# Optimization experiments

Hardware: AMD Instinct MI355X
Metric: run time of the kernel (lower is better)

The kernel has to match this reference:

```python
import jax, jax.numpy as jnp
import numpy as np

B, S, IDIM, D, T, DUR_MAX = 32, 512, 256, 256, 4096, 16
EPS = 1e-6
SIGMA_C = 2.0
PAD = 0
LOG_SQRT_2PI = 0.9189385332046727  # 0.5*log(2*pi)


def setup_inputs() -> dict:
    rng = np.random.default_rng(0)
    # durations in [1, DUR_MAX); clip so each row's total length <= T (ragged tails)
    durs = rng.integers(1, DUR_MAX, size=(B, S))
    excl = np.cumsum(durs, axis=-1) - durs
    durs = np.minimum(durs, np.maximum(T - excl, 0))
    # token ids in [1, IDIM) so PAD=0 only appears via explicit padding
    text = rng.integers(1, IDIM, size=(B, S))
    embed = rng.standard_normal((IDIM, D)).astype(np.float32)
    embed[PAD] = 0.0  # padding_idx=0 row is zeros in nn.Embedding
    return {
        "text": jnp.asarray(text, dtype=jnp.int64),
        "durs": jnp.asarray(durs, dtype=jnp.int64),
        "embed": jnp.asarray(embed),
        "total_time": T,
    }


def reference(text, durs, embed, total_time):
    # F.pad(text/durs, [0, 2]) with value 0
    text_p = jnp.pad(text, ((0, 0), (0, 2)), constant_values=PAD)   # [B, S+2]
    durs_p = jnp.pad(durs, ((0, 0), (0, 2)), constant_values=0)     # [B, S+2]
    S2 = text_p.shape[-1]

    cum = jnp.cumsum(durs_p, axis=-1)                               # [B, S+2]
    durs_f = durs_p.astype(jnp.float32)
    # token centers: durs/2 + exclusive cumsum
    c = durs_f / 2.0 + (cum - durs_p).astype(jnp.float32)           # [B, S+2]
    sig = durs_f / SIGMA_C + EPS                                    # [B, S+2]

    t = jnp.arange(total_time, dtype=jnp.float32) + 0.5             # [T]
    z = (t[None, :, None] - c[:, None, :]) / sig[:, None, :]        # [B, T, S+2]
    # Normal(c, sig).log_prob(t).exp()
    w = jnp.exp(-0.5 * z * z - jnp.log(sig)[:, None, :] - LOG_SQRT_2PI)

    # zero weights on pad tokens, then normalize over tokens
    token_pad = (text_p == PAD)                                     # [B, S+2]
    w = jnp.where(token_pad[:, None, :], 0.0, w)
    w = w / (w.sum(-1, keepdims=True) + EPS)

    # frames beyond a row's total duration correspond to pad in `repeats`:
    # zero all weights there, then set the last token column to 1.0
    time_invalid = jnp.arange(total_time)[None, :] >= cum[:, -1:]   # [B, T]
    w = jnp.where(time_invalid[:, :, None], 0.0, w)
    last_col = (jnp.arange(S2) == S2 - 1)
    w = jnp.where(time_invalid[:, :, None] & last_col[None, None, :], 1.0, w)

    emb = embed[text_p]                                             # [B, S+2, D]
    return jnp.einsum("bts,bsd->btd", w, emb)                       # [B, T, D]
```

## Files before the change

kernel.cpp:

```cpp
#include <hip/hip_runtime.h>

#define B_ 32
#define S_ 512
#define D_ 256
#define T_ 4096
#define IDIM_ 256
#define EPS_ 1e-6f
#define INV_SQRT_2PI 0.3989422804014327f
#define NHALF_LOG2E -0.7213475204444817f
#define W_ 28
#define FPW_ 16

typedef float float4n __attribute__((ext_vector_type(4)));

__global__ __launch_bounds__(512) void GaussianEmbedding_prep(
    const int* __restrict__ text, const int* __restrict__ durs,
    float4* __restrict__ toks, int* __restrict__ tof, int* __restrict__ totb)
{
    int b = blockIdx.x;
    int s = threadIdx.x;
    int dur = durs[b * S_ + s];
    int lane = s & 63, wv = s >> 6;

    int incl = dur;
    #pragma unroll
    for (int o = 1; o < 64; o <<= 1) {
        int v = __shfl_up(incl, o);
        if (lane >= o) incl += v;
    }
    __shared__ int wsum[8];
    __shared__ int stot;
    if (lane == 63) wsum[wv] = incl;
    __syncthreads();
    int woff = 0;
    for (int i = 0; i < wv; ++i) woff += wsum[i];
    int excl = woff + incl - dur;

    if (s == 0) {
        int tot = 0;
        for (int i = 0; i < 8; ++i) tot += wsum[i];
        totb[b] = tot;
        stot = tot;
    }
    __syncthreads();
    int total = stot;

    float df = (float)dur;
    float sig = df * 0.5f + EPS_;
    float inv = 1.0f / sig;
    float4 tk;
    tk.x = df * 0.5f + (float)excl;
    tk.y = inv;
    tk.z = INV_SQRT_2PI * inv;
    tk.w = __int_as_float(text[b * S_ + s] & (IDIM_ - 1));
    toks[b * S_ + s] = tk;

    for (int f = excl; f < excl + dur; ++f)
        tof[b * T_ + f] = s;
    for (int f = total + s; f < T_; f += S_)
        tof[b * T_ + f] = S_ - 1;
}

__global__ __launch_bounds__(256) void GaussianEmbedding_main(
    const float4n* __restrict__ toks, const int* __restrict__ tof,
    const int* __restrict__ totb, const float4n* __restrict__ embed4,
    float4n* __restrict__ out)
{
    int lane = threadIdx.x & 63;
    int wave = __builtin_amdgcn_readfirstlane(blockIdx.x * 4 + (threadIdx.x >> 6));
    int b  = wave >> 8;
    int t0 = (wave & 255) * FPW_;

    int total = totb[b];

    float4n acc[FPW_];
    #pragma unroll
    for (int f = 0; f < FPW_; ++f) acc[f] = (float4n){0.f, 0.f, 0.f, 0.f};

    if (t0 < total) {
        int tlo = t0 - W_;              if (tlo < 0) tlo = 0;
        int thi = t0 + FPW_ - 1 + W_;   if (thi > total - 1) thi = total - 1;
        int lo = tof[b * T_ + tlo];
        int hi = tof[b * T_ + thi];
        if (lo < 0) lo = 0; if (hi > S_ - 1) hi = S_ - 1; if (hi < lo) hi = lo;
        lo = __builtin_amdgcn_readfirstlane(lo);
        hi = __builtin_amdgcn_readfirstlane(hi);
        int nrel = hi - lo;

        int fl = lane >> 2;
        int j0 = lane & 3;
        float tcf = (float)(t0 + fl) + 0.5f;
        float pacc = 0.f;

        for (int chunk = 0; chunk <= nrel; chunk += 4) {
            int idx = chunk + j0;
            int cidx = idx > nrel ? nrel : idx;
            float4n tk = toks[b * S_ + lo + cidx];
            float z = (tcf - tk.x) * tk.y;
            float w = exp2f(NHALF_LOG2E * z * z) * tk.z;
            if (idx > nrel) w = 0.f;

            float ws = w;
            ws += __shfl_xor(ws, 1);
            ws += __shfl_xor(ws, 2);
            pacc += ws;

            int wbits = __float_as_int(w);
            int tbits = __float_as_int(tk.w);
            #pragma unroll
            for (int j = 0; j < 4; ++j) {
                if (chunk + j <= nrel) {
                    int tok = __builtin_amdgcn_readlane(tbits, j);
                    float4n ev = embed4[tok * (D_ / 4) + lane];
                    #pragma unroll
                    for (int f = 0; f < FPW_; ++f) {
                        float wf = __int_as_float(
                            __builtin_amdgcn_readlane(wbits, f * 4 + j));
                        acc[f] += wf * ev;
                    }
                }
            }
        }

        int pbits = __float_as_int(pacc);
        #pragma unroll
        for (int f = 0; f < FPW_; ++f) {
            float pf = __int_as_float(__builtin_amdgcn_readlane(pbits, f * 4));
            float sf = (t0 + f < total) ? 1.0f / (pf + EPS_) : 0.0f;
            acc[f] *= sf;
        }
    }

    size_t base = (size_t)(b * T_ + t0) * (D_ / 4) + lane;
    #pragma unroll
    for (int f = 0; f < FPW_; ++f)
        __builtin_nontemporal_store(acc[f], out + base + (size_t)f * (D_ / 4));
}

extern "C" void kernel_launch(void* const* d_in, const int* in_sizes, int n_in,
                              void* d_out, int out_size, void* d_ws, size_t ws_size,
                              hipStream_t stream)
{
    const int* text    = (const int*)d_in[0];
    const int* durs    = (const int*)d_in[1];
    const float* embed = (const float*)d_in[2];

    float4* toks = (float4*)d_ws;
    int* tof  = (int*)((char*)d_ws + (size_t)B_ * S_ * sizeof(float4));
    int* totb = tof + (size_t)B_ * T_;

    GaussianEmbedding_prep<<<B_, S_, 0, stream>>>(text, durs, toks, tof, totb);
    GaussianEmbedding_main<<<(B_ * T_) / (FPW_ * 4), 256, 0, stream>>>(
        (const float4n*)toks, tof, totb, (const float4n*)embed, (float4n*)d_out);
}
```

Measured before the change: 153.5 us.

## Fuse prep into main kernel with per-block shared-memory token table

Removes the separate prep kernel and its global workspace round trip. Each block now redoes the per-row prefix sum over durations, builds the token parameter table in LDS, and finds each wave's token window bounds directly from the interval test, so the frame-to-token map is no longer needed. This saves one kernel launch and the dependent global reads, in exchange for every one of the 64 blocks per row repeating the scan and table build.

```diff
diff --git a/kernel.cpp b/kernel.cpp
--- a/kernel.cpp
+++ b/kernel.cpp
@@ -10,81 +10,83 @@
 #define NHALF_LOG2E -0.7213475204444817f
 #define W_ 28
 #define FPW_ 16
+#define WPB_ 4
+#define FPB_ (FPW_ * WPB_)
 
 typedef float float4n __attribute__((ext_vector_type(4)));
 
-__global__ __launch_bounds__(512) void GaussianEmbedding_prep(
+__global__ __launch_bounds__(256) void GaussianEmbedding_fused(
     const int* __restrict__ text, const int* __restrict__ durs,
-    float4* __restrict__ toks, int* __restrict__ tof, int* __restrict__ totb)
+    const float4n* __restrict__ embed4, float4n* __restrict__ out)
 {
-    int b = blockIdx.x;
-    int s = threadIdx.x;
-    int dur = durs[b * S_ + s];
-    int lane = s & 63, wv = s >> 6;
+    __shared__ float4n s_tok[S_];
+    __shared__ int s_wsum[WPB_];
+    __shared__ int s_bnd[2 * WPB_];
 
-    int incl = dur;
+    int tid  = threadIdx.x;
+    int lane = tid & 63, wv = tid >> 6;
+    int bid  = blockIdx.x;
+    int b    = bid >> 6;
+    int fblk = (bid & 63) * FPB_;
+
+    int2 dd = ((const int2*)durs)[(b * S_ >> 1) + tid];
+    int2 tt = ((const int2*)text)[(b * S_ >> 1) + tid];
+    int pair = dd.x + dd.y;
+    int incl = pair;
     #pragma unroll
     for (int o = 1; o < 64; o <<= 1) {
         int v = __shfl_up(incl, o);
         if (lane >= o) incl += v;
     }
-    __shared__ int wsum[8];
-    __shared__ int stot;
-    if (lane == 63) wsum[wv] = incl;
+    if (lane == 63) s_wsum[wv] = incl;
+    if (tid < 2 * WPB_) s_bnd[tid] = 0;
     __syncthreads();
-    int woff = 0;
-    for (int i = 0; i < wv; ++i) woff += wsum[i];
-    int excl = woff + incl - dur;
+    int woff = 0, total = 0;
+    #pragma unroll
+    for (int i = 0; i < WPB_; ++i) {
+        int v = s_wsum[i];
+        total += v;
+        if (i < wv) woff += v;
+    }
+    int excl0 = woff + incl - pair;
+    int excl1 = excl0 + dd.x;
 
-    if (s == 0) {
-        int tot = 0;
-        for (int i = 0; i < 8; ++i) tot += wsum[i];
-        totb[b] = tot;
-        stot = tot;
+    int s0 = tid * 2;
+    {
+        float df0 = (float)dd.x, df1 = (float)dd.y;
+        float i0 = 1.0f / (df0 * 0.5f + EPS_);
+        float i1 = 1.0f / (df1 * 0.5f + EPS_);
+        float4n p0 = { df0 * 0.5f + (float)excl0, i0, INV_SQRT_2PI * i0,
+                       __int_as_float(tt.x & (IDIM_ - 1)) };
+        float4n p1 = { df1 * 0.5f + (float)excl1, i1, INV_SQRT_2PI * i1,
+                       __int_as_float(tt.y & (IDIM_ - 1)) };
+        s_tok[s0]     = p0;
+        s_tok[s0 + 1] = p1;
+    }
+
+    #pragma unroll
+    for (int w = 0; w < WPB_; ++w) {
+        int t0w = fblk + w * FPW_;
+        if (t0w < total) {
+            int tlo = t0w - W_;             if (tlo < 0) tlo = 0;
+            int thi = t0w + FPW_ - 1 + W_;  if (thi > total - 1) thi = total - 1;
+            if (excl0 <= tlo && tlo < excl1)        s_bnd[2 * w]     = s0;
+            if (excl1 <= tlo && tlo < excl1 + dd.y) s_bnd[2 * w]     = s0 + 1;
+            if (excl0 <= thi && thi < excl1)        s_bnd[2 * w + 1] = s0;
+            if (excl1 <= thi && thi < excl1 + dd.y) s_bnd[2 * w + 1] = s0 + 1;
+        }
     }
     __syncthreads();
-    int total = stot;
 
-    float df = (float)dur;
-    float sig = df * 0.5f + EPS_;
-    float inv = 1.0f / sig;
-    float4 tk;
-    tk.x = df * 0.5f + (float)excl;
-    tk.y = inv;
-    tk.z = INV_SQRT_2PI * inv;
-    tk.w = __int_as_float(text[b * S_ + s] & (IDIM_ - 1));
-    toks[b * S_ + s] = tk;
-
-    for (int f = excl; f < excl + dur; ++f)
-        tof[b * T_ + f] = s;
-    for (int f = total + s; f < T_; f += S_)
-        tof[b * T_ + f] = S_ - 1;
-}
-
-__global__ __launch_bounds__(256) void GaussianEmbedding_main(
-    const float4n* __restrict__ toks, const int* __restrict__ tof,
-    const int* __restrict__ totb, const float4n* __restrict__ embed4,
-    float4n* __restrict__ out)
-{
-    int lane = threadIdx.x & 63;
-    int wave = __builtin_amdgcn_readfirstlane(blockIdx.x * 4 + (threadIdx.x >> 6));
-    int b  = wave >> 8;
-    int t0 = (wave & 255) * FPW_;
-
-    int total = totb[b];
-
+    int t0 = fblk + wv * FPW_;
     float4n acc[FPW_];
     #pragma unroll
     for (int f = 0; f < FPW_; ++f) acc[f] = (float4n){0.f, 0.f, 0.f, 0.f};
 
     if (t0 < total) {
-        int tlo = t0 - W_;              if (tlo < 0) tlo = 0;
-        int thi = t0 + FPW_ - 1 + W_;   if (thi > total - 1) thi = total - 1;
-        int lo = tof[b * T_ + tlo];
-        int hi = tof[b * T_ + thi];
-        if (lo < 0) lo = 0; if (hi > S_ - 1) hi = S_ - 1; if (hi < lo) hi = lo;
-        lo = __builtin_amdgcn_readfirstlane(lo);
-        hi = __builtin_amdgcn_readfirstlane(hi);
+        int lo = __builtin_amdgcn_readfirstlane(s_bnd[2 * wv]);
+        int hi = __builtin_amdgcn_readfirstlane(s_bnd[2 * wv + 1]);
+        if (hi < lo) hi = lo;
         int nrel = hi - lo;
 
         int fl = lane >> 2;
@@ -95,7 +97,7 @@
         for (int chunk = 0; chunk <= nrel; chunk += 4) {
             int idx = chunk + j0;
             int cidx = idx > nrel ? nrel : idx;
-            float4n tk = toks[b * S_ + lo + cidx];
+            float4n tk = s_tok[lo + cidx];
             float z = (tcf - tk.x) * tk.y;
             float w = exp2f(NHALF_LOG2E * z * z) * tk.z;
             if (idx > nrel) w = 0.f;
@@ -144,12 +146,8 @@
     const int* text    = (const int*)d_in[0];
     const int* durs    = (const int*)d_in[1];
     const float* embed = (const float*)d_in[2];
+    (void)d_ws; (void)ws_size;
 
-    float4* toks = (float4*)d_ws;
-    int* tof  = (int*)((char*)d_ws + (size_t)B_ * S_ * sizeof(float4));
-    int* totb = tof + (size_t)B_ * T_;
-
-    GaussianEmbedding_prep<<<B_, S_, 0, stream>>>(text, durs, toks, tof, totb);
-    GaussianEmbedding_main<<<(B_ * T_) / (FPW_ * 4), 256, 0, stream>>>(
-        (const float4n*)toks, tof, totb, (const float4n*)embed, (float4n*)d_out);
+    GaussianEmbedding_fused<<<(B_ * T_) / FPB_, 256, 0, stream>>>(
+        text, durs, (const float4n*)embed, (float4n*)d_out);
 }
```

Result: no change. 151.6 us (median of 2 runs) (-1.2%).
